# Kernel tuning notes

Hardware: AMD Instinct MI355X
Metric: run time of the kernel (lower is better)

Reference implementation:

```python
import jax, jax.numpy as jnp
import numpy as np

NN_SIZE = 10  # matches init_kwargs nn_size


def _knn_idx(points, k):
    """points: (B,N,D). Returns (B,N,k) indices of k nearest neighbors, self excluded."""
    sq = jnp.sum(points * points, axis=-1)  # (B,N)
    # squared euclidean distances (B,N,N)
    d2 = sq[:, :, None] + sq[:, None, :] - 2.0 * jnp.einsum('bnd,bmd->bnm', points, points)
    _, idx = jax.lax.top_k(-d2, k + 1)  # smallest distances; first hit is self
    return idx[:, :, 1:]  # drop self -> (B,N,k)


def _uniform_laplacian(points, knn_idx):
    """points: (B,N,D); knn_idx: (B,N,K). lap = mean(neighbors) - point."""
    neigh = jax.vmap(lambda p, i: p[i])(points, knn_idx)  # (B,N,K,D) gather per batch
    return jnp.mean(neigh, axis=2) - points


def setup_inputs() -> dict:
    key = jax.random.key(0)
    k1, k2 = jax.random.split(key)
    B, N, D = 2, 8192, 3
    point1 = jax.random.normal(k1, (B, N, D), dtype=jnp.float32)
    point2 = jax.random.normal(k2, (B, N, D), dtype=jnp.float32)
    return {"point1": point1, "point2": point2}


def reference(point1, point2):
    knn_idx = _knn_idx(point1, NN_SIZE)          # connectivity from ref cloud
    lap1 = _uniform_laplacian(point1, knn_idx)   # (B,N,3)
    lap2 = _uniform_laplacian(point2, knn_idx)   # reuse knn_idx
    # metric = L1Loss (mean reduction); use_norm=False
    return jnp.mean(jnp.abs(lap1 - lap2))
```

## Files before the change

kernel.cpp:

```cpp
#include <hip/hip_runtime.h>
#include <math.h>


constexpr int NPTS  = 8192;
constexpr int NB    = 2;
constexpr int KNN   = 10;
constexpr int QPB   = 64;
constexpr int WPB   = 8;
constexpr int BLOCK = QPB * WPB;
constexpr int MASK13 = 0xFFFFE000;

constexpr int   G    = 32;
constexpr int   NC   = G * G * G;
constexpr float BMIN = -5.5f;
constexpr float BW   = 11.0f;
constexpr float H    = BW / G;
constexpr float INVH = (float)G / BW;

__device__ __forceinline__ void ins1(int l[KNN], int x) {
#pragma unroll
    for (int k = KNN - 1; k > 0; --k) l[k] = min(l[k], max(l[k - 1], x));
    l[0] = min(l[0], x);
}
__device__ __forceinline__ void ins2(int l[KNN], int a, int b) {
    const int b0 = min(a, b), b1 = max(a, b);
#pragma unroll
    for (int k = KNN - 1; k >= 2; --k)
        l[k] = min(l[k], min(max(l[k - 1], b0), max(l[k - 2], b1)));
    l[1] = min(l[1], min(max(l[0], b0), b1));
    l[0] = min(l[0], b0);
}

__global__ void pack_bin(const float* __restrict__ p1, float4* __restrict__ w,
                         int* __restrict__ hist, int* __restrict__ cellof) {
    const int i = blockIdx.x * blockDim.x + threadIdx.x;
    if (i >= NB * NPTS) return;
    const float x = p1[3 * i], y = p1[3 * i + 1], z = p1[3 * i + 2];
    w[i] = make_float4(x, y, z, fmaf(x, x, fmaf(y, y, z * z)));
    const int cx = min(max((int)floorf((x - BMIN) * INVH), 0), G - 1);
    const int cy = min(max((int)floorf((y - BMIN) * INVH), 0), G - 1);
    const int cz = min(max((int)floorf((z - BMIN) * INVH), 0), G - 1);
    const int c = (cz << 10) | (cy << 5) | cx;
    cellof[i] = c;
    atomicAdd(&hist[(i >> 13) * NC + c], 1);
}

__global__ __launch_bounds__(1024)
void scan_cells(const int* __restrict__ hist, int* __restrict__ starts,
                float* __restrict__ out, int* __restrict__ nfail) {
    __shared__ int part[1024];
    const int b = blockIdx.x, t = threadIdx.x;
    if (b == 0 && t == 0) { out[0] = 0.0f; nfail[0] = 0; }
    const int* hb = hist + b * NC;
    int* sb = starts + b * (NC + 1);
    const int c0 = t * 32;
    int loc[32]; int sum = 0;
#pragma unroll
    for (int j = 0; j < 32; ++j) { loc[j] = hb[c0 + j]; sum += loc[j]; }
    part[t] = sum;
    __syncthreads();
    for (int off = 1; off < 1024; off <<= 1) {
        const int v = (t >= off) ? part[t - off] : 0;
        __syncthreads();
        part[t] += v;
        __syncthreads();
    }
    int run = part[t] - sum;
#pragma unroll
    for (int j = 0; j < 32; ++j) { sb[c0 + j] = run; run += loc[j]; }
    if (t == 1023) sb[NC] = run;
}

__global__ void scatter_all(const int* __restrict__ cellof,
                            const int* __restrict__ starts,
                            int* __restrict__ hist,
                            const float4* __restrict__ w,
                            const float* __restrict__ p2,
                            float4* __restrict__ wsorted,
                            float4* __restrict__ p2s) {
    const int i = blockIdx.x * blockDim.x + threadIdx.x;
    if (i >= NB * NPTS) return;
    const int b = i >> 13;
    const int c = cellof[i];
    const int old = atomicSub(&hist[b * NC + c], 1);
    const int pos = b * NPTS + starts[b * (NC + 1) + c] + old - 1;
    wsorted[pos] = w[i];
    p2s[pos] = make_float4(p2[3 * i], p2[3 * i + 1], p2[3 * i + 2], 0.0f);
}

__global__ __launch_bounds__(BLOCK)
void phase1(const float4* __restrict__ wsorted, const float4* __restrict__ p2s,
            const int* __restrict__ starts, float* __restrict__ out,
            int* __restrict__ nfail, int* __restrict__ worklist)
{
    __shared__ int mv[WPB * KNN * QPB];

    const int batch = blockIdx.x >> 7;
    const int lane  = threadIdx.x & 63;
    const int wv    = __builtin_amdgcn_readfirstlane(threadIdx.x >> 6);
    const int qpos  = ((blockIdx.x & 127) << 6) + lane;

    const float4* W  = wsorted + batch * NPTS;
    const float4* P2 = p2s + batch * NPTS;
    const int*    st = starts + batch * (NC + 1);

    const float4 qp = W[qpos];
    const int cx = min(max((int)floorf((qp.x - BMIN) * INVH), 0), G - 1);
    const int cy = min(max((int)floorf((qp.y - BMIN) * INVH), 0), G - 1);
    const int cz = min(max((int)floorf((qp.z - BMIN) * INVH), 0), G - 1);
    const float lox = BMIN + cx * H, loy = BMIN + cy * H, loz = BMIN + cz * H;
    const float df = fminf(fminf(fminf(qp.x - lox, lox + H - qp.x),
                                 fminf(qp.y - loy, loy + H - qp.y)),
                           fminf(qp.z - loz, loz + H - qp.z));
    const float m2x = -2.0f * qp.x, m2y = -2.0f * qp.y, m2z = -2.0f * qp.z;
    const float q2 = qp.w;
    const int IMAX = 0x7FFFFFFF;

    int l[KNN];
#pragma unroll
    for (int k = 0; k < KNN; ++k) l[k] = IMAX;

#pragma unroll
    for (int r = 0; r < 9; ++r) {
        const int dy = r % 3 - 1, dz = r / 3 - 1;
        const int ay = cy + dy, az = cz + dz;
        int j0 = 0, j1 = 0;
        if ((unsigned)ay < G && (unsigned)az < G) {
            const int cbase = (az << 10) | (ay << 5);
            j0 = st[cbase + max(cx - 1, 0)];
            j1 = st[cbase + min(cx + 1, G - 1) + 1];
        }
        for (int j = j0 + wv; j < j1; j += WPB) {
            const float4 c4 = W[j];
            const float d2 = fmaf(m2x, c4.x,
                             fmaf(m2y, c4.y,
                             fmaf(m2z, c4.z, c4.w + q2)));
            int key = (__float_as_int(d2) & MASK13) | j;
            key = (j == qpos) ? IMAX : key;
            ins1(l, key);
        }
    }

#pragma unroll
    for (int k = 0; k < KNN; ++k) mv[(wv * KNN + k) * QPB + lane] = l[k];
    __syncthreads();

    if (threadIdx.x < QPB) {
        int M[KNN];
#pragma unroll
        for (int k = 0; k < KNN; ++k) M[k] = IMAX;
#pragma unroll 4
        for (int e = 0; e < WPB * KNN; e += 2)
            ins2(M, mv[e * QPB + lane], mv[(e + 1) * QPB + lane]);

        const float tau = __int_as_float(M[KNN - 1] & MASK13);
        const float R = H + df;
        const bool covered = (tau <= R * R * 0.996f);
        float v = 0.0f;
        if (covered) {
            float s1x = 0, s1y = 0, s1z = 0, s2x = 0, s2y = 0, s2z = 0;
#pragma unroll
            for (int k = 0; k < KNN; ++k) {
                const int j = M[k] & (NPTS - 1);
                const float4 c4 = W[j];
                const float4 n2 = P2[j];
                s1x += c4.x; s1y += c4.y; s1z += c4.z;
                s2x += n2.x; s2y += n2.y; s2z += n2.z;
            }
            const float4 p2v = P2[qpos];
            const float dx = (s1x * 0.1f - qp.x) - (s2x * 0.1f - p2v.x);
            const float dy2 = (s1y * 0.1f - qp.y) - (s2y * 0.1f - p2v.y);
            const float dz2 = (s1z * 0.1f - qp.z) - (s2z * 0.1f - p2v.z);
            v = fabsf(dx) + fabsf(dy2) + fabsf(dz2);
        } else {
            const int wi = atomicAdd(nfail, 1);
            worklist[wi] = (batch << 16) | qpos;
        }
#pragma unroll
        for (int off = 32; off >= 1; off >>= 1) v += __shfl_down(v, off);
        if (threadIdx.x == 0)
            atomicAdd(out, v * (1.0f / (float)(NB * NPTS * 3)));
    }
}

__global__ __launch_bounds__(BLOCK)
void phase2(const float4* __restrict__ wsorted, const float4* __restrict__ p2s,
            const int* __restrict__ nfail, const int* __restrict__ worklist,
            float* __restrict__ out)
{
    __shared__ float bsum;
    if (threadIdx.x == 0) bsum = 0.0f;
    __syncthreads();

    const int lane = threadIdx.x & 63;
    const int wv   = threadIdx.x >> 6;
    const int wid  = blockIdx.x * WPB + wv;
    const int NW   = gridDim.x * WPB;
    const int nf   = *nfail;
    const int IMAX = 0x7FFFFFFF;
    float acc = 0.0f;

    for (int i = wid; i < nf; i += NW) {
        const int e = worklist[i];
        const int batch = e >> 16, qpos = e & 0xFFFF;
        const float4* W  = wsorted + batch * NPTS;
        const float4* P2 = p2s + batch * NPTS;
        const float4 qp = W[qpos];
        const float m2x = -2.0f * qp.x, m2y = -2.0f * qp.y, m2z = -2.0f * qp.z;
        const float q2 = qp.w;

        int l[KNN];
#pragma unroll
        for (int k = 0; k < KNN; ++k) l[k] = IMAX;

#pragma unroll 2
        for (int it = 0; it < NPTS / 128; ++it) {
            const int ja = it * 128 + lane, jb = ja + 64;
            const float4 ca = W[ja];
            const float4 cb = W[jb];
            const float da = fmaf(m2x, ca.x, fmaf(m2y, ca.y, fmaf(m2z, ca.z, ca.w + q2)));
            const float db = fmaf(m2x, cb.x, fmaf(m2y, cb.y, fmaf(m2z, cb.z, cb.w + q2)));
            int ka = (__float_as_int(da) & MASK13) | ja;
            int kb = (__float_as_int(db) & MASK13) | jb;
            ka = (ja == qpos) ? IMAX : ka;
            kb = (jb == qpos) ? IMAX : kb;
            ins2(l, ka, kb);
        }
        for (int off = 1; off < 64; off <<= 1) {
            int p[KNN];
#pragma unroll
            for (int k = 0; k < KNN; ++k) p[k] = __shfl_xor(l[k], off);
            ins2(l, p[0], p[1]); ins2(l, p[2], p[3]); ins2(l, p[4], p[5]);
            ins2(l, p[6], p[7]); ins2(l, p[8], p[9]);
        }
        float s1x = 0, s1y = 0, s1z = 0, s2x = 0, s2y = 0, s2z = 0;
#pragma unroll
        for (int k = 0; k < KNN; ++k) {
            const int j = l[k] & (NPTS - 1);
            const float4 c4 = W[j];
            const float4 n2 = P2[j];
            s1x += c4.x; s1y += c4.y; s1z += c4.z;
            s2x += n2.x; s2y += n2.y; s2z += n2.z;
        }
        const float4 p2v = P2[qpos];
        const float dx = (s1x * 0.1f - qp.x) - (s2x * 0.1f - p2v.x);
        const float dy = (s1y * 0.1f - qp.y) - (s2y * 0.1f - p2v.y);
        const float dz = (s1z * 0.1f - qp.z) - (s2z * 0.1f - p2v.z);
        if (lane == 0) acc += fabsf(dx) + fabsf(dy) + fabsf(dz);
    }

    if (lane == 0 && acc != 0.0f) atomicAdd(&bsum, acc);
    __syncthreads();
    if (threadIdx.x == 0 && bsum != 0.0f)
        atomicAdd(out, bsum * (1.0f / (float)(NB * NPTS * 3)));
}

constexpr int CHUNK = NPTS / WPB;

__global__ void prep_pack(const float* __restrict__ p, float4* __restrict__ w) {
    const int i = blockIdx.x * blockDim.x + threadIdx.x;
    if (i < NB * NPTS) {
        const float x = p[3 * i], y = p[3 * i + 1], z = p[3 * i + 2];
        w[i] = make_float4(x, y, z, fmaf(x, x, fmaf(y, y, z * z)));
    }
}

__global__ __launch_bounds__(BLOCK, 2)
void knn_lap(const float4* __restrict__ w1, const float* __restrict__ p2,
             float* __restrict__ out)
{
    __shared__ int mv[WPB * KNN * QPB];
    const int batch = blockIdx.x >> 7;
    const int qbase = (blockIdx.x & 127) << 6;
    const int lane  = threadIdx.x & 63;
    const int wv    = __builtin_amdgcn_readfirstlane(threadIdx.x >> 6);
    const int query = qbase + lane;
    const float4* Wb = w1 + batch * NPTS;
    const float4 qp = Wb[query];
    const float m2x = -2.0f * qp.x, m2y = -2.0f * qp.y, m2z = -2.0f * qp.z;
    const float q2 = qp.w;
    const int IMAX = 0x7FFFFFFF;
    int l[KNN];
#pragma unroll
    for (int k = 0; k < KNN; ++k) l[k] = IMAX;
    const int c0 = wv * CHUNK;
    const float4* cand = Wb + c0;
#pragma unroll 4
    for (int i = 0; i < CHUNK; i += 2) {
        const float4 ca = cand[i];
        const float4 cb = cand[i + 1];
        const int ja = c0 + i, jb = ja + 1;
        const float da = fmaf(m2x, ca.x, fmaf(m2y, ca.y, fmaf(m2z, ca.z, ca.w + q2)));
        const float db = fmaf(m2x, cb.x, fmaf(m2y, cb.y, fmaf(m2z, cb.z, cb.w + q2)));
        int ka = (__float_as_int(da) & MASK13) | ja;
        int kb = (__float_as_int(db) & MASK13) | jb;
        ka = (ja == query) ? IMAX : ka;
        kb = (jb == query) ? IMAX : kb;
        ins2(l, ka, kb);
    }
#pragma unroll
    for (int k = 0; k < KNN; ++k) mv[(wv * KNN + k) * QPB + lane] = l[k];
    __syncthreads();
    if (threadIdx.x < QPB) {
        int m[KNN];
#pragma unroll
        for (int k = 0; k < KNN; ++k) m[k] = IMAX;
#pragma unroll 4
        for (int e = 0; e < WPB * KNN; e += 2)
            ins2(m, mv[e * QPB + lane], mv[(e + 1) * QPB + lane]);
        const float* P2b = p2 + (size_t)batch * NPTS * 3;
        float s1x = 0, s1y = 0, s1z = 0, s2x = 0, s2y = 0, s2z = 0;
#pragma unroll
        for (int k = 0; k < KNN; ++k) {
            const int j = m[k] & (NPTS - 1);
            const float4 c = Wb[j];
            s1x += c.x; s1y += c.y; s1z += c.z;
            s2x += P2b[3 * j + 0]; s2y += P2b[3 * j + 1]; s2z += P2b[3 * j + 2];
        }
        const int q = qbase + threadIdx.x;
        const float p2x = P2b[3 * q + 0], p2y = P2b[3 * q + 1], p2z = P2b[3 * q + 2];
        const float dx = (s1x * 0.1f - qp.x) - (s2x * 0.1f - p2x);
        const float dy = (s1y * 0.1f - qp.y) - (s2y * 0.1f - p2y);
        const float dz = (s1z * 0.1f - qp.z) - (s2z * 0.1f - p2z);
        float v = fabsf(dx) + fabsf(dy) + fabsf(dz);
#pragma unroll
        for (int off = 32; off >= 1; off >>= 1) v += __shfl_down(v, off);
        if (threadIdx.x == 0)
            atomicAdd(out, v * (1.0f / (float)(NB * NPTS * 3)));
    }
}

extern "C" void kernel_launch(void* const* d_in, const int* in_sizes, int n_in,
                              void* d_out, int out_size, void* d_ws, size_t ws_size,
                              hipStream_t stream) {
    const float* p1 = (const float*)d_in[0];
    const float* p2 = (const float*)d_in[1];
    float* out = (float*)d_out;

    size_t off = 0;
    float4* w       = (float4*)d_ws;               off += (size_t)NB * NPTS * 16;
    int*    hist    = (int*)((char*)d_ws + off);   off += (size_t)NB * NC * 4;
    int*    starts  = (int*)((char*)d_ws + off);   off += (size_t)NB * (NC + 1) * 4 + 8;
    int*    cellof  = (int*)((char*)d_ws + off);   off += (size_t)NB * NPTS * 4;
    float4* wsorted = (float4*)((char*)d_ws + off); off += (size_t)NB * NPTS * 16;
    float4* p2s     = (float4*)((char*)d_ws + off); off += (size_t)NB * NPTS * 16;
    int*    nfail   = (int*)((char*)d_ws + off);   off += 16;
    int*    worklist= (int*)((char*)d_ws + off);   off += (size_t)NB * NPTS * 4;

    if (ws_size < off) {
        hipMemsetAsync(out, 0, sizeof(float), stream);
        prep_pack<<<(NB * NPTS + 255) / 256, 256, 0, stream>>>(p1, w);
        knn_lap<<<NB * (NPTS / QPB), BLOCK, 0, stream>>>(w, p2, out);
        return;
    }

    hipMemsetAsync(hist, 0, (size_t)NB * NC * 4, stream);
    pack_bin<<<(NB * NPTS + 255) / 256, 256, 0, stream>>>(p1, w, hist, cellof);
    scan_cells<<<NB, 1024, 0, stream>>>(hist, starts, out, nfail);
    scatter_all<<<(NB * NPTS + 255) / 256, 256, 0, stream>>>(cellof, starts, hist,
                                                             w, p2, wsorted, p2s);
    phase1<<<NB * (NPTS / QPB), BLOCK, 0, stream>>>(wsorted, p2s, starts, out,
                                                    nfail, worklist);
    phase2<<<256, BLOCK, 0, stream>>>(wsorted, p2s, nfail, worklist, out);
}
```

Baseline: 131.1 us.

## Widen grid search for outlier queries, warp-scan cells, cheaper sorted merges, retune phase2

Phase1 searches a 5x5x5 cell window for queries far from the origin (large squared norm) and a 3x3x3 window otherwise, with the coverage radius scaled to match. The goal is fewer sparse outlier queries falling back to the slow brute-force phase2. The cell-prefix scan replaces a 1024-step shared-memory Hillis-Steele loop with wavefront shuffle scans. Top-K merges now exploit the sorted lists through a staged pairwise insert, and phase2 moves to smaller blocks with direct global atomics. In exchange, the wider window costs more distance work per outlier query, and the variable-trip loop can diverge within a wavefront.

Result: faster. 122.8 us (-6.3%).

```diff
diff --git a/kernel.cpp b/kernel.cpp
--- a/kernel.cpp
+++ b/kernel.cpp
@@ -29,6 +29,22 @@
         l[k] = min(l[k], min(max(l[k - 1], b0), max(l[k - 2], b1)));
     l[1] = min(l[1], min(max(l[0], b0), b1));
     l[0] = min(l[0], b0);
+}
+template<int S>
+__device__ __forceinline__ void ins2s(int l[KNN], int a, int b) {
+    const int b0 = min(a, b), b1 = max(a, b);
+#pragma unroll
+    for (int k = KNN - 1; k >= S + 2; --k)
+        l[k] = min(l[k], min(max(l[k - 1], b0), max(l[k - 2], b1)));
+    l[S + 1] = min(l[S + 1], min(max(l[S], b0), b1));
+    l[S] = min(l[S], b0);
+}
+__device__ __forceinline__ void merge_sorted(int l[KNN], const int p[KNN]) {
+    ins2s<0>(l, p[0], p[1]);
+    ins2s<2>(l, p[2], p[3]);
+    ins2s<4>(l, p[4], p[5]);
+    ins2s<6>(l, p[6], p[7]);
+    ins2s<8>(l, p[8], p[9]);
 }
 
 __global__ void pack_bin(const float* __restrict__ p1, float4* __restrict__ w,
@@ -48,7 +64,7 @@
 __global__ __launch_bounds__(1024)
 void scan_cells(const int* __restrict__ hist, int* __restrict__ starts,
                 float* __restrict__ out, int* __restrict__ nfail) {
-    __shared__ int part[1024];
+    __shared__ int wsum[16];
     const int b = blockIdx.x, t = threadIdx.x;
     if (b == 0 && t == 0) { out[0] = 0.0f; nfail[0] = 0; }
     const int* hb = hist + b * NC;
@@ -57,15 +73,27 @@
     int loc[32]; int sum = 0;
 #pragma unroll
     for (int j = 0; j < 32; ++j) { loc[j] = hb[c0 + j]; sum += loc[j]; }
-    part[t] = sum;
+    const int lane = t & 63, wv = t >> 6;
+    int incl = sum;
+#pragma unroll
+    for (int off = 1; off < 64; off <<= 1) {
+        const int v = __shfl_up(incl, off);
+        if (lane >= off) incl += v;
+    }
+    if (lane == 63) wsum[wv] = incl;
     __syncthreads();
-    for (int off = 1; off < 1024; off <<= 1) {
-        const int v = (t >= off) ? part[t - off] : 0;
-        __syncthreads();
-        part[t] += v;
-        __syncthreads();
-    }
-    int run = part[t] - sum;
+    if (t < 16) {
+        const int v = wsum[t];
+        int iv = v;
+#pragma unroll
+        for (int off = 1; off < 16; off <<= 1) {
+            const int u = __shfl_up(iv, off);
+            if (t >= off) iv += u;
+        }
+        wsum[t] = iv - v;
+    }
+    __syncthreads();
+    int run = wsum[wv] + incl - sum;
 #pragma unroll
     for (int j = 0; j < 32; ++j) { sb[c0 + j] = run; run += loc[j]; }
     if (t == 1023) sb[NC] = run;
@@ -116,28 +144,33 @@
     const float q2 = qp.w;
     const int IMAX = 0x7FFFFFFF;
 
+    const int s  = (q2 > 4.8f) ? 2 : 1;
+    const int Wd = 2 * s + 1;
+    const int runs = Wd * Wd;
+
     int l[KNN];
 #pragma unroll
     for (int k = 0; k < KNN; ++k) l[k] = IMAX;
 
-#pragma unroll
-    for (int r = 0; r < 9; ++r) {
-        const int dy = r % 3 - 1, dz = r / 3 - 1;
-        const int ay = cy + dy, az = cz + dz;
-        int j0 = 0, j1 = 0;
-        if ((unsigned)ay < G && (unsigned)az < G) {
-            const int cbase = (az << 10) | (ay << 5);
-            j0 = st[cbase + max(cx - 1, 0)];
-            j1 = st[cbase + min(cx + 1, G - 1) + 1];
-        }
-        for (int j = j0 + wv; j < j1; j += WPB) {
-            const float4 c4 = W[j];
-            const float d2 = fmaf(m2x, c4.x,
-                             fmaf(m2y, c4.y,
-                             fmaf(m2z, c4.z, c4.w + q2)));
-            int key = (__float_as_int(d2) & MASK13) | j;
-            key = (j == qpos) ? IMAX : key;
-            ins1(l, key);
+    for (int r = 0; r < 25; ++r) {
+        if (r < runs) {
+            const int dy = r % Wd - s, dz = r / Wd - s;
+            const int ay = cy + dy, az = cz + dz;
+            int j0 = 0, j1 = 0;
+            if ((unsigned)ay < G && (unsigned)az < G) {
+                const int cbase = (az << 10) | (ay << 5);
+                j0 = st[cbase + max(cx - s, 0)];
+                j1 = st[cbase + min(cx + s, G - 1) + 1];
+            }
+            for (int j = j0 + wv; j < j1; j += WPB) {
+                const float4 c4 = W[j];
+                const float d2 = fmaf(m2x, c4.x,
+                                 fmaf(m2y, c4.y,
+                                 fmaf(m2z, c4.z, c4.w + q2)));
+                int key = (__float_as_int(d2) & MASK13) | j;
+                key = (j == qpos) ? IMAX : key;
+                ins1(l, key);
+            }
         }
     }
 
@@ -149,12 +182,16 @@
         int M[KNN];
 #pragma unroll
         for (int k = 0; k < KNN; ++k) M[k] = IMAX;
-#pragma unroll 4
-        for (int e = 0; e < WPB * KNN; e += 2)
-            ins2(M, mv[e * QPB + lane], mv[(e + 1) * QPB + lane]);
+#pragma unroll
+        for (int e = 0; e < WPB; ++e) {
+            int p[KNN];
+#pragma unroll
+            for (int k = 0; k < KNN; ++k) p[k] = mv[(e * KNN + k) * QPB + lane];
+            merge_sorted(M, p);
+        }
 
         const float tau = __int_as_float(M[KNN - 1] & MASK13);
-        const float R = H + df;
+        const float R = (float)s * H + df;
         const bool covered = (tau <= R * R * 0.996f);
         float v = 0.0f;
         if (covered) {
@@ -183,19 +220,18 @@
     }
 }
 
-__global__ __launch_bounds__(BLOCK)
+constexpr int P2BLK = 256;
+constexpr int P2GRID = 512;
+
+__global__ __launch_bounds__(P2BLK)
 void phase2(const float4* __restrict__ wsorted, const float4* __restrict__ p2s,
             const int* __restrict__ nfail, const int* __restrict__ worklist,
             float* __restrict__ out)
 {
-    __shared__ float bsum;
-    if (threadIdx.x == 0) bsum = 0.0f;
-    __syncthreads();
-
     const int lane = threadIdx.x & 63;
     const int wv   = threadIdx.x >> 6;
-    const int wid  = blockIdx.x * WPB + wv;
-    const int NW   = gridDim.x * WPB;
+    const int wid  = blockIdx.x * (P2BLK / 64) + wv;
+    const int NW   = P2GRID * (P2BLK / 64);
     const int nf   = *nfail;
     const int IMAX = 0x7FFFFFFF;
     float acc = 0.0f;
@@ -230,8 +266,7 @@
             int p[KNN];
 #pragma unroll
             for (int k = 0; k < KNN; ++k) p[k] = __shfl_xor(l[k], off);
-            ins2(l, p[0], p[1]); ins2(l, p[2], p[3]); ins2(l, p[4], p[5]);
-            ins2(l, p[6], p[7]); ins2(l, p[8], p[9]);
+            merge_sorted(l, p);
         }
         float s1x = 0, s1y = 0, s1z = 0, s2x = 0, s2y = 0, s2z = 0;
 #pragma unroll
@@ -249,10 +284,8 @@
         if (lane == 0) acc += fabsf(dx) + fabsf(dy) + fabsf(dz);
     }
 
-    if (lane == 0 && acc != 0.0f) atomicAdd(&bsum, acc);
-    __syncthreads();
-    if (threadIdx.x == 0 && bsum != 0.0f)
-        atomicAdd(out, bsum * (1.0f / (float)(NB * NPTS * 3)));
+    if (lane == 0 && acc != 0.0f)
+        atomicAdd(out, acc * (1.0f / (float)(NB * NPTS * 3)));
 }
 
 constexpr int CHUNK = NPTS / WPB;
@@ -305,9 +338,13 @@
         int m[KNN];
 #pragma unroll
         for (int k = 0; k < KNN; ++k) m[k] = IMAX;
-#pragma unroll 4
-        for (int e = 0; e < WPB * KNN; e += 2)
-            ins2(m, mv[e * QPB + lane], mv[(e + 1) * QPB + lane]);
+#pragma unroll
+        for (int e = 0; e < WPB; ++e) {
+            int p[KNN];
+#pragma unroll
+            for (int k = 0; k < KNN; ++k) p[k] = mv[(e * KNN + k) * QPB + lane];
+            merge_sorted(m, p);
+        }
         const float* P2b = p2 + (size_t)batch * NPTS * 3;
         float s1x = 0, s1y = 0, s1z = 0, s2x = 0, s2y = 0, s2z = 0;
 #pragma unroll
@@ -361,5 +398,5 @@
                                                              w, p2, wsorted, p2s);
     phase1<<<NB * (NPTS / QPB), BLOCK, 0, stream>>>(wsorted, p2s, starts, out,
                                                     nfail, worklist);
-    phase2<<<256, BLOCK, 0, stream>>>(wsorted, p2s, nfail, worklist, out);
-}
+    phase2<<<P2GRID, P2BLK, 0, stream>>>(wsorted, p2s, nfail, worklist, out);
+}
```
